# Optimization experiments

Measured on AMD Instinct MI355X. Metric: run time of the kernel, lower is better.

The kernel has to match this reference:

```python
import jax, jax.numpy as jnp
import numpy as np

VOCAB = 50257
EMB = 256
HID = 256
FORGET_BIAS = 1.0


def setup_inputs() -> dict:
    key = jax.random.key(0)
    ks = jax.random.split(key, 8)
    B, T = 16, 256
    s = 0.05
    return {
        "tokens": jax.random.randint(ks[0], (B, T), 0, VOCAB, dtype=jnp.int32),
        # embedding matrix init mimics tf.random_uniform(-1, 1)
        "emb": jax.random.uniform(ks[1], (VOCAB, EMB), jnp.float32, -1.0, 1.0),
        "W1": jax.random.normal(ks[2], (EMB + HID, 4 * HID), jnp.float32) * s,
        "b1": jnp.zeros((4 * HID,), jnp.float32),
        "W2": jax.random.normal(ks[3], (HID + HID, 4 * HID), jnp.float32) * s,
        "b2": jnp.zeros((4 * HID,), jnp.float32),
        "Wout": jax.random.normal(ks[4], (HID, VOCAB), jnp.float32) * s,
        "bout": jnp.zeros((VOCAB,), jnp.float32),
    }


def _lstm_cell(c, h, x, W, b):
    # BasicLSTMCell: gates = [x, h] @ W + b, split i, j, f, o
    g = jnp.concatenate([x, h], axis=-1) @ W + b
    i, j, f, o = jnp.split(g, 4, axis=-1)
    c_new = c * jax.nn.sigmoid(f + FORGET_BIAS) + jax.nn.sigmoid(i) * jnp.tanh(j)
    h_new = jnp.tanh(c_new) * jax.nn.sigmoid(o)
    return c_new, h_new


def reference(tokens, emb, W1, b1, W2, b2, Wout, bout):
    B, T = tokens.shape
    x = emb[tokens]                 # [B, T, EMB] embedding lookup
    x_tm = jnp.swapaxes(x, 0, 1)    # [T, B, EMB] time-major for scan

    def step(carry, xt):
        c1, h1, c2, h2 = carry
        c1, h1 = _lstm_cell(c1, h1, xt, W1, b1)
        c2, h2 = _lstm_cell(c2, h2, h1, W2, b2)
        return (c1, h1, c2, h2), h2

    z = jnp.zeros((B, HID), x.dtype)
    _, hs = jax.lax.scan(step, (z, z, z, z), x_tm)  # hs: [T, B, HID]
    hs = jnp.swapaxes(hs, 0, 1).reshape(-1, HID)    # [B*T, HID] (batch-major flatten as in tf.reshape)
    logits = hs @ Wout + bout                        # [B*T, VOCAB]
    return logits
```

## Files before the change

### kernel.cpp

```cpp
#include <hip/hip_runtime.h>
#include <hip/hip_bf16.h>
#include <stdint.h>

#define BB 16
#define TT 256
#define HH 256
#define EE 256
#define GG 1024
#define VV 50257
#define NN 4096

typedef unsigned short u16;
typedef __attribute__((ext_vector_type(8))) short short8;
typedef __attribute__((ext_vector_type(4))) float f32x4;

__device__ __forceinline__ float sigm(float x){
    float e = __builtin_amdgcn_exp2f(fminf(-x*1.44269504f, 60.0f));
    return 1.0f/(1.0f+e);
}
__device__ __forceinline__ float tanha(float x){
    float e = __builtin_amdgcn_exp2f(fminf(x*2.885390082f, 60.0f));
    return (e-1.0f)/(e+1.0f);
}
__device__ __forceinline__ u16 f2bf(float f){
    uint32_t u = __float_as_uint(f);
    u = (u + 0x7FFFu + ((u>>16)&1u)) >> 16;
    return (u16)u;
}
__device__ __forceinline__ void st32_coh(uint32_t* p, uint32_t v){
    __hip_atomic_store(p, v, __ATOMIC_RELAXED, __HIP_MEMORY_SCOPE_AGENT);
}
__device__ __forceinline__ uint32_t poll_pair(const uint32_t* p){
    uint32_t v = __hip_atomic_load(p, __ATOMIC_RELAXED, __HIP_MEMORY_SCOPE_AGENT);
    while ((v & 0xFFFFu) == 0xFFFFu || (v >> 16) == 0xFFFFu){
        __builtin_amdgcn_s_sleep(1);
        v = __hip_atomic_load(p, __ATOMIC_RELAXED, __HIP_MEMORY_SCOPE_AGENT);
    }
    return v;
}
__device__ __forceinline__ void gl_lds16(const void* g, void* s){
    __builtin_amdgcn_global_load_lds((const __attribute__((address_space(1))) unsigned int*)g,
                                     (__attribute__((address_space(3))) unsigned int*)s, 16, 0, 0);
}

__global__ __launch_bounds__(256) void g1_kernel(const int* __restrict__ tok, const float* __restrict__ emb,
                                                 const float* __restrict__ W1, const float* __restrict__ b1,
                                                 float* __restrict__ G1t){
    __shared__ float xs[64*64];
    __shared__ float wsm[64*64];
    int n0 = blockIdx.x * 64;
    int g0 = blockIdx.y * 64;
    int tid = threadIdx.x;
    int sl = tid & 63;
    int kk = (tid >> 6) * 16;
    int mytok = tok[n0 + sl];
    float acc[4][4] = {};
    int ni = tid & 15, gi = tid >> 4;
    for (int kc = 0; kc < 4; ++kc){
        int k0 = kc*64;
        __syncthreads();
        #pragma unroll
        for (int i4 = 0; i4 < 4; ++i4){
            float4 xv = *(const float4*)(&emb[(size_t)mytok*EE + k0 + kk + i4*4]);
            xs[(kk+i4*4+0)*64 + sl] = xv.x;
            xs[(kk+i4*4+1)*64 + sl] = xv.y;
            xs[(kk+i4*4+2)*64 + sl] = xv.z;
            xs[(kk+i4*4+3)*64 + sl] = xv.w;
        }
        #pragma unroll
        for (int i = 0; i < 16; ++i){
            wsm[(kk+i)*64 + sl] = W1[(size_t)(k0+kk+i)*GG + g0 + sl];
        }
        __syncthreads();
        for (int k = 0; k < 64; ++k){
            float4 av = *(const float4*)(&xs[k*64 + ni*4]);
            float4 bv = *(const float4*)(&wsm[k*64 + gi*4]);
            float a_[4] = {av.x, av.y, av.z, av.w};
            float b_[4] = {bv.x, bv.y, bv.z, bv.w};
            #pragma unroll
            for (int i = 0; i < 4; ++i)
                #pragma unroll
                for (int j = 0; j < 4; ++j)
                    acc[i][j] += a_[i]*b_[j];
        }
    }
    #pragma unroll
    for (int i = 0; i < 4; ++i){
        int n = n0 + ni*4 + i;
        int b = n >> 8;
        int tt_ = n & 255;
        float4 o;
        o.x = acc[i][0] + b1[g0+gi*4+0];
        o.y = acc[i][1] + b1[g0+gi*4+1];
        o.z = acc[i][2] + b1[g0+gi*4+2];
        o.w = acc[i][3] + b1[g0+gi*4+3];
        *(float4*)(&G1t[(size_t)(tt_*16 + b)*GG + g0 + gi*4]) = o;
    }
}

__global__ __launch_bounds__(1024) void persist_kernel(
        const float* __restrict__ G1t, const float* __restrict__ W1,
        const float* __restrict__ W2, const float* __restrict__ b2,
        const float* __restrict__ Wout, u16* __restrict__ WoutT,
        u16* __restrict__ h1y, u16* __restrict__ h2b){
    __shared__ __align__(16) char smem[12288];
    const int bid = blockIdx.x;
    const int tid = threadIdx.x;

    if (bid >= 96){
        u16* tile = (u16*)smem;
        const int r = tid >> 4, i = tid & 15;
        for (int tau = bid - 96; tau < 786*4; tau += 128){
            int ky = tau / 786;
            int nx = tau - ky*786;
            int n0 = nx*64, k0 = ky*64;
            #pragma unroll
            for (int jj = 0; jj < 4; ++jj){
                int n = n0 + i*4 + jj;
                float f = (n < VV) ? Wout[(size_t)(k0 + r)*VV + n] : 0.0f;
                tile[(i*4 + jj)*66 + r] = f2bf(f);
            }
            __syncthreads();
            {
                int kl = i*4;
                uint2 v;
                v.x = (uint32_t)tile[r*66 + kl+0] | ((uint32_t)tile[r*66 + kl+1] << 16);
                v.y = (uint32_t)tile[r*66 + kl+2] | ((uint32_t)tile[r*66 + kl+3] << 16);
                *(uint2*)(&WoutT[(size_t)(n0 + r)*256 + k0 + kl]) = v;
            }
            __syncthreads();
        }
        return;
    }

    const int g  = bid & 7;
    const int rr = bid >> 3;
    const int l  = tid & 63;
    const int wv = tid >> 6;
    uint32_t* h1y32 = (uint32_t*)h1y;
    uint32_t* h2b32 = (uint32_t*)h2b;

    if (rr < 4){
        const int r1 = rr;
        const int gate = wv >> 2, usub = wv & 3;
        const int colw = gate*HH + 64*r1 + 16*usub;
        short8 wf[8];
        {
            const int col = colw + (l & 15);
            const int kb = (l >> 4) << 3;
            #pragma unroll
            for (int kk = 0; kk < 8; ++kk){
                short8 s;
                #pragma unroll
                for (int j = 0; j < 8; ++j)
                    s[j] = (short)f2bf(W1[(size_t)(HH + kk*32 + kb + j)*GG + col]);
                wf[kk] = s;
            }
        }
        u16*      hA   = (u16*)smem;
        uint32_t* hA32 = (uint32_t*)smem;
        float*    gm   = (float*)(smem + 1024);
        const int ab = tid >> 5, ap_ = tid & 31;
        float creg0 = 0.f, creg1 = 0.f;

        for (int t = 0; t < TT; ++t){
            float c0 = 0.f, c1 = 0.f;
            if (l < 16){
                c0 = G1t[((size_t)t*BB + 2*g + 0)*GG + colw + l];
                c1 = G1t[((size_t)t*BB + 2*g + 1)*GG + colw + l];
            }
            f32x4 acc = {c0, c1, 0.f, 0.f};
            if (t > 0){
                if (tid < 256){
                    int b = tid >> 7, p = tid & 127;
                    hA32[b*128 + p] = poll_pair(&h1y32[(((size_t)(t-1)*8 + g)*2 + b)*128 + p]);
                }
                __syncthreads();
                const u16* app = hA + (l & 1)*256 + ((l >> 4) << 3);
                f32x4 acc2 = {0.f, 0.f, 0.f, 0.f};
                #pragma unroll
                for (int kk = 0; kk < 4; ++kk){
                    acc  = __builtin_amdgcn_mfma_f32_16x16x32_bf16(*(const short8*)(app + (2*kk  )*32), wf[2*kk  ], acc , 0, 0, 0);
                    acc2 = __builtin_amdgcn_mfma_f32_16x16x32_bf16(*(const short8*)(app + (2*kk+1)*32), wf[2*kk+1], acc2, 0, 0, 0);
                }
                acc[0] += acc2[0];
                acc[1] += acc2[1];
            }
            if (l < 16){
                gm[(gate*64 + usub*16 + l)*2 + 0] = acc[0];
                gm[(gate*64 + usub*16 + l)*2 + 1] = acc[1];
            }
            __syncthreads();
            if (tid < 64){
                int u0 = 2*ap_, u1 = 2*ap_ + 1;
                float gi0 = gm[(0*64 + u0)*2 + ab], gi1 = gm[(0*64 + u1)*2 + ab];
                float gj0 = gm[(1*64 + u0)*2 + ab], gj1 = gm[(1*64 + u1)*2 + ab];
                float gf0 = gm[(2*64 + u0)*2 + ab], gf1 = gm[(2*64 + u1)*2 + ab];
                float go0 = gm[(3*64 + u0)*2 + ab], go1 = gm[(3*64 + u1)*2 + ab];
                float cn0 = creg0 * sigm(gf0 + 1.0f) + sigm(gi0)*tanha(gj0);
                float cn1 = creg1 * sigm(gf1 + 1.0f) + sigm(gi1)*tanha(gj1);
                float hn0 = tanha(cn0)*sigm(go0);
                float hn1 = tanha(cn1)*sigm(go1);
                creg0 = cn0; creg1 = cn1;
                uint32_t pk = (uint32_t)f2bf(hn0) | ((uint32_t)f2bf(hn1) << 16);
                st32_coh(&h1y32[(((size_t)t*8 + g)*2 + ab)*128 + 32*r1 + ap_], pk);
            }
            __syncthreads();
        }
    } else {
        const int r2 = rr - 4;
        const int nt = wv >> 1, kh = wv & 1;
        const int gate = nt >> 1, usub = nt & 1;
        const int colw = gate*HH + 32*r2 + 16*usub;
        short8 wf[8];
        {
            const int col = colw + (l & 15);
            const int kb = (l >> 4) << 3;
            #pragma unroll
            for (int kk = 0; kk < 8; ++kk){
                short8 s;
                #pragma unroll
                for (int j = 0; j < 8; ++j)
                    s[j] = (short)f2bf(W2[(size_t)(kh*256 + kk*32 + kb + j)*GG + col]);
                wf[kk] = s;
            }
        }
        u16*      uB   = (u16*)smem;
        uint32_t* uB32 = (uint32_t*)smem;
        float*    gm   = (float*)(smem + 2048);
        const int ab = tid >> 4, ap_ = tid & 15;
        float creg0 = 0.f, creg1 = 0.f;
        float bvs[4][2];
        if (tid < 32){
            #pragma unroll
            for (int gg = 0; gg < 4; ++gg){
                bvs[gg][0] = b2[gg*HH + 32*r2 + 2*ap_];
                bvs[gg][1] = b2[gg*HH + 32*r2 + 2*ap_ + 1];
            }
        }

        for (int tt = 0; tt < TT; ++tt){
            if (tid < 512){
                int b = tid >> 8, q = tid & 255;
                uint32_t v;
                if (q < 128)
                    v = poll_pair(&h1y32[(((size_t)tt*8 + g)*2 + b)*128 + q]);
                else if (tt > 0)
                    v = poll_pair(&h2b32[((size_t)(2*g + b)*TT + (tt-1))*128 + (q - 128)]);
                else
                    v = 0;
                uB32[b*256 + q] = v;
            }
            __syncthreads();
            f32x4 acc = {0.f, 0.f, 0.f, 0.f};
            f32x4 acc2 = {0.f, 0.f, 0.f, 0.f};
            const u16* app = uB + (l & 1)*512 + kh*256 + ((l >> 4) << 3);
            #pragma unroll
            for (int kk = 0; kk < 4; ++kk){
                acc  = __builtin_amdgcn_mfma_f32_16x16x32_bf16(*(const short8*)(app + (2*kk  )*32), wf[2*kk  ], acc , 0, 0, 0);
                acc2 = __builtin_amdgcn_mfma_f32_16x16x32_bf16(*(const short8*)(app + (2*kk+1)*32), wf[2*kk+1], acc2, 0, 0, 0);
            }
            acc[0] += acc2[0];
            acc[1] += acc2[1];
            if (l < 16){
                gm[((gate*32 + usub*16 + l)*2 + 0)*2 + kh] = acc[0];
                gm[((gate*32 + usub*16 + l)*2 + 1)*2 + kh] = acc[1];
            }
            __syncthreads();
            if (tid < 32){
                int u0 = 2*ap_, u1 = 2*ap_ + 1;
                float gi0 = gm[((0*32 + u0)*2 + ab)*2 + 0] + gm[((0*32 + u0)*2 + ab)*2 + 1] + bvs[0][0];
                float gi1 = gm[((0*32 + u1)*2 + ab)*2 + 0] + gm[((0*32 + u1)*2 + ab)*2 + 1] + bvs[0][1];
                float gj0 = gm[((1*32 + u0)*2 + ab)*2 + 0] + gm[((1*32 + u0)*2 + ab)*2 + 1] + bvs[1][0];
                float gj1 = gm[((1*32 + u1)*2 + ab)*2 + 0] + gm[((1*32 + u1)*2 + ab)*2 + 1] + bvs[1][1];
                float gf0 = gm[((2*32 + u0)*2 + ab)*2 + 0] + gm[((2*32 + u0)*2 + ab)*2 + 1] + bvs[2][0];
                float gf1 = gm[((2*32 + u1)*2 + ab)*2 + 0] + gm[((2*32 + u1)*2 + ab)*2 + 1] + bvs[2][1];
                float go0 = gm[((3*32 + u0)*2 + ab)*2 + 0] + gm[((3*32 + u0)*2 + ab)*2 + 1] + bvs[3][0];
                float go1 = gm[((3*32 + u1)*2 + ab)*2 + 0] + gm[((3*32 + u1)*2 + ab)*2 + 1] + bvs[3][1];
                float cn0 = creg0 * sigm(gf0 + 1.0f) + sigm(gi0)*tanha(gj0);
                float cn1 = creg1 * sigm(gf1 + 1.0f) + sigm(gi1)*tanha(gj1);
                float hn0 = tanha(cn0)*sigm(go0);
                float hn1 = tanha(cn1)*sigm(go1);
                creg0 = cn0; creg1 = cn1;
                uint32_t pk = (uint32_t)f2bf(hn0) | ((uint32_t)f2bf(hn1) << 16);
                st32_coh(&h2b32[((size_t)(2*g + ab)*TT + tt)*128 + 16*r2 + ap_], pk);
            }
            __syncthreads();
        }
    }
}

__global__ __launch_bounds__(256) void out_gemm(const u16* __restrict__ A, const u16* __restrict__ Bt,
                                                const float* __restrict__ bout, float* __restrict__ out){
    __shared__ __align__(16) u16 lds[2][2][8192];
    const int bid = blockIdx.x;
    const int x   = bid & 7;
    const int wgl = bid >> 3;
    const int mb  = x*4 + (wgl & 3);
    const int nb  = wgl >> 2;
    const int m0 = mb*128, n0 = nb*128;
    const int tid = threadIdx.x;
    const int l = tid & 63;
    const int wv = tid >> 6;
    const int wm = wv >> 1, wn = wv & 1;
    const int lr = l & 15, lh = l >> 4;

    f32x4 acc[4][4];
    #pragma unroll
    for (int mf = 0; mf < 4; ++mf)
        #pragma unroll
        for (int nf = 0; nf < 4; ++nf) acc[mf][nf] = (f32x4){0.f,0.f,0.f,0.f};

    #define STAGE(c, k0) { \
        _Pragma("unroll") \
        for (int j = 0; j < 4; ++j){ \
            int f = j*256 + tid; \
            int row = f >> 3; \
            int kps = (f & 7) ^ (row & 7); \
            gl_lds16(A  + (size_t)(m0+row)*256 + (k0) + kps*8, (char*)&lds[c][0][0] + f*16); \
            gl_lds16(Bt + (size_t)(n0+row)*256 + (k0) + kps*8, (char*)&lds[c][1][0] + f*16); \
        } }

    STAGE(0, 0)
    __syncthreads();
    #pragma unroll
    for (int ks = 0; ks < 4; ++ks){
        const int cur = ks & 1;
        if (ks < 3) STAGE(cur^1, (ks+1)*64)
        const char* ab = (const char*)&lds[cur][0][0];
        const char* bbp = (const char*)&lds[cur][1][0];
        #pragma unroll
        for (int ksub = 0; ksub < 2; ++ksub){
            short8 af[4], bf[4];
            const int kp = ksub*4 + lh;
            #pragma unroll
            for (int mf = 0; mf < 4; ++mf){
                int row = wm*64 + mf*16 + lr;
                af[mf] = *(const short8*)(ab + row*128 + ((kp ^ (row&7)) << 4));
            }
            #pragma unroll
            for (int nf = 0; nf < 4; ++nf){
                int row = wn*64 + nf*16 + lr;
                bf[nf] = *(const short8*)(bbp + row*128 + ((kp ^ (row&7)) << 4));
            }
            #pragma unroll
            for (int mf = 0; mf < 4; ++mf)
                #pragma unroll
                for (int nf = 0; nf < 4; ++nf)
                    acc[mf][nf] = __builtin_amdgcn_mfma_f32_16x16x32_bf16(af[mf], bf[nf], acc[mf][nf], 0, 0, 0);
        }
        __syncthreads();
    }
    #undef STAGE

    float* ldsF = (float*)&lds[0][0][0];
    #pragma unroll
    for (int nf = 0; nf < 4; ++nf){
        int col = wn*64 + nf*16 + lr;
        int gcol = n0 + col;
        float bb2 = (gcol < VV) ? bout[gcol] : 0.0f;
        #pragma unroll
        for (int mf = 0; mf < 4; ++mf)
            #pragma unroll
            for (int r = 0; r < 4; ++r){
                int row = wm*64 + mf*16 + lh*4 + r;
                ldsF[row*128 + col] = acc[mf][nf][r] + bb2;
            }
    }
    __syncthreads();
    #pragma unroll
    for (int j = 0; j < 16; ++j){
        int f = j*256 + tid;
        int row = f >> 5;
        int c4 = (f & 31)*4;
        int gcol = n0 + c4;
        float4 v = *(const float4*)(ldsF + row*128 + c4);
        if (gcol + 3 < VV){
            *(float4*)(&out[(size_t)(m0+row)*VV + gcol]) = v;
        } else {
            #pragma unroll
            for (int e = 0; e < 4; ++e)
                if (gcol + e < VV) out[(size_t)(m0+row)*VV + gcol + e] = ((const float*)&v)[e];
        }
    }
}

extern "C" void kernel_launch(void* const* d_in, const int* in_sizes, int n_in,
                              void* d_out, int out_size, void* d_ws, size_t ws_size,
                              hipStream_t stream) {
    const int*   tok  = (const int*)d_in[0];
    const float* emb  = (const float*)d_in[1];
    const float* W1   = (const float*)d_in[2];
    const float* b1   = (const float*)d_in[3];
    const float* W2   = (const float*)d_in[4];
    const float* b2   = (const float*)d_in[5];
    const float* Wout = (const float*)d_in[6];
    const float* bout = (const float*)d_in[7];
    float* out = (float*)d_out;
    char* ws = (char*)d_ws;

    u16*   h1y   = (u16*)  (ws);
    u16*   h2b   = (u16*)  (ws + 2097152);
    float* G1t   = (float*)(ws + 4194304);
    u16*   WoutT = (u16*)  (ws + 4194304 + 16777216);

    hipMemsetAsync(ws, 0xFF, 4194304, stream);
    g1_kernel<<<dim3(64, 16), 256, 0, stream>>>(tok, emb, W1, b1, G1t);
    persist_kernel<<<224, 1024, 0, stream>>>(G1t, W1, W2, b2, Wout, WoutT, h1y, h2b);
    out_gemm<<<12576, 256, 0, stream>>>(h2b, WoutT, bout, out);
}
```

Measured before the change: 798.9 us.

## Single-buffer output GEMM LDS and split epilogue to raise occupancy

Drops double-buffered LDS staging in the output GEMM in favor of a single buffer loaded synchronously each k-step. The epilogue is split into two half-tile passes with a padded row stride of 132 floats. Together these cut shared memory to 36KB and request 4 blocks per CU via launch bounds. The aim is more resident workgroups to hide global latency in this store-bound GEMM. The cost is losing overlap between the next tile load and the MFMAs, plus extra barriers in the epilogue.

```diff
diff --git a/kernel.cpp b/kernel.cpp
--- a/kernel.cpp
+++ b/kernel.cpp
@@ -290,9 +290,12 @@
     }
 }
 
-__global__ __launch_bounds__(256) void out_gemm(const u16* __restrict__ A, const u16* __restrict__ Bt,
-                                                const float* __restrict__ bout, float* __restrict__ out){
-    __shared__ __align__(16) u16 lds[2][2][8192];
+__global__ __launch_bounds__(256, 4) void out_gemm(const u16* __restrict__ A, const u16* __restrict__ Bt,
+                                                   const float* __restrict__ bout, float* __restrict__ out){
+    __shared__ __align__(16) char smem[36864];
+    u16* ldsA = (u16*)smem;
+    u16* ldsB = (u16*)(smem + 16384);
+    float* ldsF = (float*)smem;
     const int bid = blockIdx.x;
     const int x   = bid & 7;
     const int wgl = bid >> 3;
@@ -311,24 +314,17 @@
         #pragma unroll
         for (int nf = 0; nf < 4; ++nf) acc[mf][nf] = (f32x4){0.f,0.f,0.f,0.f};
 
-    #define STAGE(c, k0) { \
-        _Pragma("unroll") \
-        for (int j = 0; j < 4; ++j){ \
-            int f = j*256 + tid; \
-            int row = f >> 3; \
-            int kps = (f & 7) ^ (row & 7); \
-            gl_lds16(A  + (size_t)(m0+row)*256 + (k0) + kps*8, (char*)&lds[c][0][0] + f*16); \
-            gl_lds16(Bt + (size_t)(n0+row)*256 + (k0) + kps*8, (char*)&lds[c][1][0] + f*16); \
-        } }
-
-    STAGE(0, 0)
-    __syncthreads();
     #pragma unroll
     for (int ks = 0; ks < 4; ++ks){
-        const int cur = ks & 1;
-        if (ks < 3) STAGE(cur^1, (ks+1)*64)
-        const char* ab = (const char*)&lds[cur][0][0];
-        const char* bbp = (const char*)&lds[cur][1][0];
+        #pragma unroll
+        for (int j = 0; j < 4; ++j){
+            int f = j*256 + tid;
+            int row = f >> 3;
+            int kps = (f & 7) ^ (row & 7);
+            gl_lds16(A  + (size_t)(m0+row)*256 + ks*64 + kps*8, (char*)ldsA + f*16);
+            gl_lds16(Bt + (size_t)(n0+row)*256 + ks*64 + kps*8, (char*)ldsB + f*16);
+        }
+        __syncthreads();
         #pragma unroll
         for (int ksub = 0; ksub < 2; ++ksub){
             short8 af[4], bf[4];
@@ -336,12 +332,12 @@
             #pragma unroll
             for (int mf = 0; mf < 4; ++mf){
                 int row = wm*64 + mf*16 + lr;
-                af[mf] = *(const short8*)(ab + row*128 + ((kp ^ (row&7)) << 4));
+                af[mf] = *(const short8*)((const char*)ldsA + row*128 + ((kp ^ (row&7)) << 4));
             }
             #pragma unroll
             for (int nf = 0; nf < 4; ++nf){
                 int row = wn*64 + nf*16 + lr;
-                bf[nf] = *(const short8*)(bbp + row*128 + ((kp ^ (row&7)) << 4));
+                bf[nf] = *(const short8*)((const char*)ldsB + row*128 + ((kp ^ (row&7)) << 4));
             }
             #pragma unroll
             for (int mf = 0; mf < 4; ++mf)
@@ -351,37 +347,39 @@
         }
         __syncthreads();
     }
-    #undef STAGE
-
-    float* ldsF = (float*)&lds[0][0][0];
-    #pragma unroll
-    for (int nf = 0; nf < 4; ++nf){
-        int col = wn*64 + nf*16 + lr;
-        int gcol = n0 + col;
-        float bb2 = (gcol < VV) ? bout[gcol] : 0.0f;
-        #pragma unroll
-        for (int mf = 0; mf < 4; ++mf)
-            #pragma unroll
-            for (int r = 0; r < 4; ++r){
-                int row = wm*64 + mf*16 + lh*4 + r;
-                ldsF[row*128 + col] = acc[mf][nf][r] + bb2;
-            }
-    }
-    __syncthreads();
-    #pragma unroll
-    for (int j = 0; j < 16; ++j){
-        int f = j*256 + tid;
-        int row = f >> 5;
-        int c4 = (f & 31)*4;
-        int gcol = n0 + c4;
-        float4 v = *(const float4*)(ldsF + row*128 + c4);
-        if (gcol + 3 < VV){
-            *(float4*)(&out[(size_t)(m0+row)*VV + gcol]) = v;
-        } else {
-            #pragma unroll
-            for (int e = 0; e < 4; ++e)
-                if (gcol + e < VV) out[(size_t)(m0+row)*VV + gcol + e] = ((const float*)&v)[e];
-        }
+
+    for (int h = 0; h < 2; ++h){
+        if (wm == h){
+            #pragma unroll
+            for (int nf = 0; nf < 4; ++nf){
+                int col = wn*64 + nf*16 + lr;
+                int gcol = n0 + col;
+                float bb2 = (gcol < VV) ? bout[gcol] : 0.0f;
+                #pragma unroll
+                for (int mf = 0; mf < 4; ++mf)
+                    #pragma unroll
+                    for (int r = 0; r < 4; ++r)
+                        ldsF[(mf*16 + lh*4 + r)*132 + col] = acc[mf][nf][r] + bb2;
+            }
+        }
+        __syncthreads();
+        #pragma unroll
+        for (int j = 0; j < 8; ++j){
+            int f = j*256 + tid;
+            int row = f >> 5;
+            int c4 = (f & 31)*4;
+            int gcol = n0 + c4;
+            f32x4 v = *(const f32x4*)(ldsF + row*132 + c4);
+            int grow = m0 + h*64 + row;
+            if (gcol + 3 < VV){
+                *(f32x4*)(&out[(size_t)grow*VV + gcol]) = v;
+            } else {
+                #pragma unroll
+                for (int e = 0; e < 4; ++e)
+                    if (gcol + e < VV) out[(size_t)grow*VV + gcol + e] = v[e];
+            }
+        }
+        __syncthreads();
     }
 }
 
```

After: 773.7 us. -3.2%, faster.
